# Performance work log

Hardware: AMD Instinct MI355X
Metric: run time of the kernel (lower is better)

The kernel has to match this reference:

```python
import jax, jax.numpy as jnp
import numpy as np

NPERSEG = 128  # filter_size


def setup_inputs() -> dict:
    key = jax.random.key(0)
    x = jax.random.normal(key, (32, 64, 16384), dtype=jnp.float32)
    return {"x": x}


def _welch_psd(x):
    # window=None -> rectangular, scaling = sum(ones^2) = NPERSEG, fs = 1.0
    step = NPERSEG // 2          # noverlap = nperseg // 2
    T = x.shape[-1]
    num_segments = (T - step) // step
    # frame the signal: [B, C, S, NPERSEG]
    idx = jnp.arange(num_segments)[:, None] * step + jnp.arange(NPERSEG)
    segs = x[..., idx]
    segs = segs - jnp.mean(segs, axis=-1, keepdims=True)
    seg_fft = jnp.fft.rfft(segs, axis=-1)
    psd = (jnp.abs(seg_fft) ** 2) / NPERSEG
    # nperseg even -> double all bins except DC and Nyquist
    factor = jnp.ones((psd.shape[-1],), dtype=psd.dtype).at[1:-1].set(2.0)
    psd = psd * factor
    return jnp.mean(psd, axis=-2)  # average over segments -> [B, C, F]


def reference(x):
    psd = _welch_psd(x)                       # [B, C, F], F = 65
    F_bins = psd.shape[-1]
    sqrt_psd = jnp.sqrt(psd)
    # weights = 1 / F (faithful to original: divides by psd.shape[-1])
    barycenter = jnp.sum(sqrt_psd / F_bins, axis=0) ** 2   # [C, F] (first_iter)
    D = jnp.sqrt(barycenter)[None] / sqrt_psd              # [B, C, F]
    H = jnp.fft.irfft(D, axis=-1)                          # [B, C, 2*(F-1)=128]
    H = jnp.fft.fftshift(H, axes=-1)
    H = jnp.flip(H, axis=-1)
    B, C, T = x.shape
    K = H.shape[-1]
    # per-sample depthwise conv1d, padding='same' (torch even-kernel: left=(K-1)//2, right=K-1-left)
    left = (K - 1) // 2
    out = jax.lax.conv_general_dilated(
        x.reshape(1, B * C, T),
        H.reshape(B * C, 1, K),
        window_strides=(1,),
        padding=[(left, K - 1 - left)],
        feature_group_count=B * C,
    )
    return out.reshape(B, C, T)
```

## Files before the change

kernel.cpp:

```cpp
#include <hip/hip_runtime.h>
#include <math.h>

#define NCH   2048
#define TLEN  16384
#define NSEG  255
#define NF    65

typedef __attribute__((ext_vector_type(8))) short bf16x8;
typedef __attribute__((ext_vector_type(4))) float f32x4;

__device__ __forceinline__ unsigned short f2bf(float f) {
    union { float f; unsigned u; } v; v.f = f;
    unsigned r = v.u + 0x7FFF + ((v.u >> 16) & 1);
    return (unsigned short)(r >> 16);
}
__device__ __forceinline__ float bf2f(unsigned short b) {
    union { unsigned u; float f; } v; v.u = ((unsigned)b) << 16;
    return v.f;
}

__device__ __forceinline__ int swzA(int i) {
    return (i & ~63) | ((i & 63) ^ ((i >> 6) & 31));
}
__host__ __device__ constexpr int br6(int i) {
    return ((i & 1) << 5) | ((i & 2) << 3) | ((i & 4) << 1) |
           ((i & 8) >> 1) | ((i & 16) >> 3) | ((i & 32) >> 5);
}

__attribute__((amdgpu_flat_work_group_size(256, 256), amdgpu_waves_per_eu(2, 2)))
__global__ void psd_kernel(const float* __restrict__ x, float* __restrict__ psd_g) {
    __shared__ float xl[TLEN];
    const int ch  = blockIdx.x;
    const int tid = threadIdx.x;
    const int lane = tid & 63;
    const int w    = tid >> 6;
    const float4* __restrict__ x4 = reinterpret_cast<const float4*>(x) + (size_t)ch * (TLEN / 4);
#pragma unroll
    for (int it = 0; it < 16; ++it) {
        int i4 = it * 256 + tid;
        float4 v = x4[i4];
        int i = i4 << 2;
        xl[swzA(i + 0)] = v.x;
        xl[swzA(i + 1)] = v.y;
        xl[swzA(i + 2)] = v.z;
        xl[swzA(i + 3)] = v.w;
    }
    __syncthreads();

    const int   seg   = (tid < NSEG) ? tid : (NSEG - 1);
    const float valid = (tid < NSEG) ? 1.0f : 0.0f;
    const int   base  = seg * 64;

    float zr[64], zi[64];
#pragma unroll
    for (int i = 0; i < 64; ++i) {
        const int rb = br6(i);
        zr[i] = xl[swzA(base + 2 * rb)];
        zi[i] = xl[swzA(base + 2 * rb + 1)];
    }

    constexpr float STR[6] = {-1.0f, 0.0f, 0.70710678f, 0.92387953f, 0.98078528f, 0.99518473f};
    constexpr float STI[6] = {0.0f, -1.0f, -0.70710678f, -0.38268343f, -0.19509032f, -0.09801714f};
#pragma unroll
    for (int st = 0; st < 6; ++st) {
        const int m = 1 << st;
        float wr = 1.0f, wi = 0.0f;
#pragma unroll
        for (int j = 0; j < m; ++j) {
#pragma unroll
            for (int k = 0; k < 64; k += 2 * m) {
                const int a = k + j, b = a + m;
                float tr = wr * zr[b] - wi * zi[b];
                float ti = wr * zi[b] + wi * zr[b];
                zr[b] = zr[a] - tr; zi[b] = zi[a] - ti;
                zr[a] += tr;        zi[a] += ti;
            }
            float nwr = wr * STR[st] - wi * STI[st];
            wi = wr * STI[st] + wi * STR[st];
            wr = nwr;
        }
    }

    float vals[64];
    float p64;
    const float INV128 = 1.0f / 128.0f;
    {
        float v0 = zr[0] + zi[0];
        vals[0] = v0 * v0 * INV128 * valid;
        float v1 = zr[0] - zi[0];
        p64 = v1 * v1 * INV128 * valid;
        vals[32] = (zr[32] * zr[32] + zi[32] * zi[32]) * (2.0f * INV128) * valid;
    }
    float Wr = 0.9987954562f, Wi = -0.0490676743f;
#pragma unroll
    for (int k = 1; k < 32; ++k) {
        float ar = 0.5f * (zr[k] + zr[64 - k]);
        float ai = 0.5f * (zi[k] - zi[64 - k]);
        float br_ = 0.5f * (zi[k] + zi[64 - k]);
        float bi_ = 0.5f * (zr[64 - k] - zr[k]);
        float tr = Wr * br_ - Wi * bi_;
        float ti = Wr * bi_ + Wi * br_;
        float e1r = ar + tr, e1i = ai + ti;
        float e2r = ar - tr, e2i = ai - ti;
        vals[k]      = (e1r * e1r + e1i * e1i) * (2.0f * INV128) * valid;
        vals[64 - k] = (e2r * e2r + e2i * e2i) * (2.0f * INV128) * valid;
        float nWr = Wr * 0.9987954562f - Wi * (-0.0490676743f);
        Wi = Wr * (-0.0490676743f) + Wi * 0.9987954562f;
        Wr = nWr;
    }

    const int l = lane;
#define RSTAGE(m)                                                    \
    {                                                                \
        const bool hi = (l & (m)) != 0;                              \
        _Pragma("unroll")                                            \
        for (int j = 0; j < (m); ++j) {                              \
            float a = vals[j], b = vals[j + (m)];                    \
            float t = __shfl_xor(hi ? a : b, (m));                   \
            vals[j] = (hi ? b : a) + t;                              \
        }                                                            \
    }
    RSTAGE(32) RSTAGE(16) RSTAGE(8) RSTAGE(4) RSTAGE(2) RSTAGE(1)
#undef RSTAGE
    p64 += __shfl_xor(p64, 32);
    p64 += __shfl_xor(p64, 16);
    p64 += __shfl_xor(p64, 8);
    p64 += __shfl_xor(p64, 4);
    p64 += __shfl_xor(p64, 2);
    p64 += __shfl_xor(p64, 1);

    __syncthreads();
    float* red = xl;
    red[w * 80 + lane] = vals[0];
    if (lane == 0) red[320 + w] = p64;
    __syncthreads();
    if (tid < NF) {
        float s;
        if (tid < 64) s = red[tid] + red[80 + tid] + red[160 + tid] + red[240 + tid];
        else          s = red[320] + red[321] + red[322] + red[323];
        psd_g[ch * NF + tid] = s;
    }
}

__launch_bounds__(256)
__global__ void sqrtp_kernel(const float* __restrict__ psd_g, float* __restrict__ sqrtP,
                             float* __restrict__ S) {
    int id = blockIdx.x * 256 + threadIdx.x;
    if (id >= 64 * NF) return;
    int c = id / NF, f = id - c * NF;
    float sum = 0.0f;
    for (int b = 0; b < 32; ++b) {
        int ch = (b << 6) + c;
        float sp = sqrtf(psd_g[ch * NF + f] * (1.0f / 255.0f));
        sqrtP[ch * NF + f] = sp;
        sum += sp;
    }
    S[id] = sum * (1.0f / 65.0f);
}

__launch_bounds__(128)
__global__ void filt_kernel(const float* __restrict__ sqrtP, const float* __restrict__ S,
                            float* __restrict__ h2g) {
    __shared__ float Dl[NF];
    const int ch = blockIdx.x;
    const int c  = ch & 63;
    const int n  = threadIdx.x;
    if (n < NF) {
        if (n == 0) {
            Dl[0] = 32.0f / 65.0f;
        } else {
            float sp = sqrtP[ch * NF + n];
            float sv = S[c * NF + n];
            Dl[n] = (sp > 0.0f) ? sv / sp : 0.0f;
        }
    }
    __syncthreads();
    float sum = Dl[0] + ((n & 1) ? -Dl[64] : Dl[64]);
#pragma unroll
    for (int f = 1; f < 64; ++f) {
        int m = (f * n) & 127;
        sum += 2.0f * Dl[f] * cosf((float)m * 0.04908738521f);
    }
    float h = sum * (1.0f / 128.0f);
    h2g[ch * 128 + ((n + 63) & 127)] = h;
}

#define BS    4096
#define KPAD  160
#define XU    (BS + KPAD)
#define PHYS(u) ((u) + (((u) >> 4) << 2))

__attribute__((amdgpu_flat_work_group_size(256, 256), amdgpu_waves_per_eu(4, 4)))
__global__ void conv_kernel(const float* __restrict__ x, const float* __restrict__ h2g,
                            float* __restrict__ out) {
    __shared__ __align__(16) unsigned short Xh[PHYS(XU)];
    __shared__ __align__(16) unsigned short Xl[PHYS(XU)];
    const int bid  = blockIdx.x;
    const int ch   = bid >> 2;
    const int t0   = (bid & 3) * BS;
    const int tid  = threadIdx.x;
    const int lane = tid & 63;
    const int w    = tid >> 6;
    const float* __restrict__ xrow = x + (size_t)ch * TLEN;

    bf16x8 Ah[5], Al[5];
    {
        const float* __restrict__ hrow = h2g + ch * 128;
        const int r  = lane & 15;
        const int kg = (lane >> 4) << 2;
#pragma unroll
        for (int c = 0; c < 5; ++c) {
#pragma unroll
            for (int e = 0; e < 8; ++e) {
                int idx = 32 * c + kg + (e & 3) + ((e >> 2) << 4) - r - 1;
                float hv = (idx >= 0 && idx < 128) ? hrow[idx] : 0.0f;
                unsigned short hh = f2bf(hv);
                Ah[c][e] = (short)hh;
                Al[c][e] = (short)f2bf(hv - bf2f(hh));
            }
        }
    }

    for (int i4 = tid; i4 < XU / 4; i4 += 256) {
        int u0  = i4 << 2;
        int src = t0 - 64 + u0;
        float4 v;
        if (src >= 0 && src + 3 < TLEN) {
            v = *reinterpret_cast<const float4*>(xrow + src);
        } else {
            v.x = (src + 0 >= 0 && src + 0 < TLEN) ? xrow[src + 0] : 0.0f;
            v.y = (src + 1 >= 0 && src + 1 < TLEN) ? xrow[src + 1] : 0.0f;
            v.z = (src + 2 >= 0 && src + 2 < TLEN) ? xrow[src + 2] : 0.0f;
            v.w = (src + 3 >= 0 && src + 3 < TLEN) ? xrow[src + 3] : 0.0f;
        }
        ushort4 hi, lo;
        hi.x = f2bf(v.x); lo.x = f2bf(v.x - bf2f(hi.x));
        hi.y = f2bf(v.y); lo.y = f2bf(v.y - bf2f(hi.y));
        hi.z = f2bf(v.z); lo.z = f2bf(v.z - bf2f(hi.z));
        hi.w = f2bf(v.w); lo.w = f2bf(v.w - bf2f(hi.w));
        int p = PHYS(u0);
        *reinterpret_cast<ushort4*>(Xh + p) = hi;
        *reinterpret_cast<ushort4*>(Xl + p) = lo;
    }
    __syncthreads();

    const int ub0 = 16 * (lane & 15) + ((lane >> 4) << 2);
#pragma unroll
    for (int q = 0; q < 4; ++q) {
        const int tb = 256 * (w + (q << 2));
        f32x4 acc = {0.0f, 0.0f, 0.0f, 0.0f};
#pragma unroll
        for (int c = 0; c < 5; ++c) {
            int p0 = PHYS(ub0 + tb + 32 * c);
            ushort4 h0 = *reinterpret_cast<const ushort4*>(Xh + p0);
            ushort4 h1 = *reinterpret_cast<const ushort4*>(Xh + p0 + 20);
            ushort4 l0 = *reinterpret_cast<const ushort4*>(Xl + p0);
            ushort4 l1 = *reinterpret_cast<const ushort4*>(Xl + p0 + 20);
            bf16x8 bh = {(short)h0.x, (short)h0.y, (short)h0.z, (short)h0.w,
                         (short)h1.x, (short)h1.y, (short)h1.z, (short)h1.w};
            bf16x8 bl = {(short)l0.x, (short)l0.y, (short)l0.z, (short)l0.w,
                         (short)l1.x, (short)l1.y, (short)l1.z, (short)l1.w};
            acc = __builtin_amdgcn_mfma_f32_16x16x32_bf16(Ah[c], bh, acc, 0, 0, 0);
            acc = __builtin_amdgcn_mfma_f32_16x16x32_bf16(Ah[c], bl, acc, 0, 0, 0);
            acc = __builtin_amdgcn_mfma_f32_16x16x32_bf16(Al[c], bh, acc, 0, 0, 0);
        }
        float* orow = out + (size_t)ch * TLEN + t0 + tb
                    + 16 * (lane & 15) + ((lane >> 4) << 2);
        *reinterpret_cast<float4*>(orow) = make_float4(acc[0], acc[1], acc[2], acc[3]);
    }
}

extern "C" void kernel_launch(void* const* d_in, const int* in_sizes, int n_in,
                              void* d_out, int out_size, void* d_ws, size_t ws_size,
                              hipStream_t stream) {
    (void)in_sizes; (void)n_in; (void)out_size; (void)ws_size;
    const float* x = (const float*)d_in[0];
    float* out = (float*)d_out;
    char* ws = (char*)d_ws;
    float* psd_g = (float*)(ws);
    float* sqrtP = (float*)(ws + 532480);
    float* S     = (float*)(ws + 1064960);
    float* h2g   = (float*)(ws + 1081600);

    psd_kernel <<<NCH,     256, 0, stream>>>(x, psd_g);
    sqrtp_kernel<<<17,     256, 0, stream>>>(psd_g, sqrtP, S);
    filt_kernel<<<NCH,     128, 0, stream>>>(sqrtP, S, h2g);
    conv_kernel<<<NCH * 4, 256, 0, stream>>>(x, h2g, out);
}
```

Measured before the change: 292.6 us.

## Fuse sqrt/barycenter into filter kernel, use cosine table, vectorize LDS ops

Removes the separate sqrtp kernel launch: each filter block recomputes the per-column barycenter sum over 32 batches directly from the PSD buffer. The inverse-DFT loop now reads a shared-memory cosine table instead of calling cosf 63 times per thread. The PSD kernel's LDS stores and loads become float2 accesses with lane swaps that preserve the existing swizzle. This trades a kernel launch and an intermediate buffer for redundant sqrt work in every block (32x per bin).

```diff
diff --git a/kernel.cpp b/kernel.cpp
--- a/kernel.cpp
+++ b/kernel.cpp
@@ -29,7 +29,7 @@
 
 __attribute__((amdgpu_flat_work_group_size(256, 256), amdgpu_waves_per_eu(2, 2)))
 __global__ void psd_kernel(const float* __restrict__ x, float* __restrict__ psd_g) {
-    __shared__ float xl[TLEN];
+    __shared__ __align__(16) float xl[TLEN];
     const int ch  = blockIdx.x;
     const int tid = threadIdx.x;
     const int lane = tid & 63;
@@ -39,11 +39,13 @@
     for (int it = 0; it < 16; ++it) {
         int i4 = it * 256 + tid;
         float4 v = x4[i4];
-        int i = i4 << 2;
-        xl[swzA(i + 0)] = v.x;
-        xl[swzA(i + 1)] = v.y;
-        xl[swzA(i + 2)] = v.z;
-        xl[swzA(i + 3)] = v.w;
+        int i  = i4 << 2;
+        int a0 = swzA(i);
+        const bool sw = ((i >> 6) & 1) != 0;
+        float2 p0 = sw ? make_float2(v.y, v.x) : make_float2(v.x, v.y);
+        float2 p1 = sw ? make_float2(v.w, v.z) : make_float2(v.z, v.w);
+        *reinterpret_cast<float2*>(&xl[a0 & ~1])       = p0;
+        *reinterpret_cast<float2*>(&xl[(a0 ^ 2) & ~1]) = p1;
     }
     __syncthreads();
 
@@ -55,8 +57,11 @@
 #pragma unroll
     for (int i = 0; i < 64; ++i) {
         const int rb = br6(i);
-        zr[i] = xl[swzA(base + 2 * rb)];
-        zi[i] = xl[swzA(base + 2 * rb + 1)];
+        int a = swzA(base + 2 * rb);
+        const float2 v = *reinterpret_cast<const float2*>(&xl[a & ~1]);
+        const bool sw = ((seg ^ i) & 1) != 0;
+        zr[i] = sw ? v.y : v.x;
+        zi[i] = sw ? v.x : v.y;
     }
 
     constexpr float STR[6] = {-1.0f, 0.0f, 0.70710678f, 0.92387953f, 0.98078528f, 0.99518473f};
@@ -142,44 +147,31 @@
     }
 }
 
-__launch_bounds__(256)
-__global__ void sqrtp_kernel(const float* __restrict__ psd_g, float* __restrict__ sqrtP,
-                             float* __restrict__ S) {
-    int id = blockIdx.x * 256 + threadIdx.x;
-    if (id >= 64 * NF) return;
-    int c = id / NF, f = id - c * NF;
-    float sum = 0.0f;
-    for (int b = 0; b < 32; ++b) {
-        int ch = (b << 6) + c;
-        float sp = sqrtf(psd_g[ch * NF + f] * (1.0f / 255.0f));
-        sqrtP[ch * NF + f] = sp;
-        sum += sp;
-    }
-    S[id] = sum * (1.0f / 65.0f);
-}
-
 __launch_bounds__(128)
-__global__ void filt_kernel(const float* __restrict__ sqrtP, const float* __restrict__ S,
-                            float* __restrict__ h2g) {
+__global__ void filt_kernel(const float* __restrict__ psd_g, float* __restrict__ h2g) {
     __shared__ float Dl[NF];
+    __shared__ float cosT[128];
     const int ch = blockIdx.x;
     const int c  = ch & 63;
     const int n  = threadIdx.x;
+    cosT[n] = cosf((float)n * 0.04908738521f);
     if (n < NF) {
         if (n == 0) {
             Dl[0] = 32.0f / 65.0f;
         } else {
-            float sp = sqrtP[ch * NF + n];
-            float sv = S[c * NF + n];
-            Dl[n] = (sp > 0.0f) ? sv / sp : 0.0f;
+            float sp = sqrtf(psd_g[ch * NF + n] * (1.0f / 255.0f));
+            float s = 0.0f;
+            for (int b = 0; b < 32; ++b)
+                s += sqrtf(psd_g[((b << 6) + c) * NF + n] * (1.0f / 255.0f));
+            s *= (1.0f / 65.0f);
+            Dl[n] = (sp > 0.0f) ? s / sp : 0.0f;
         }
     }
     __syncthreads();
     float sum = Dl[0] + ((n & 1) ? -Dl[64] : Dl[64]);
 #pragma unroll
     for (int f = 1; f < 64; ++f) {
-        int m = (f * n) & 127;
-        sum += 2.0f * Dl[f] * cosf((float)m * 0.04908738521f);
+        sum += 2.0f * Dl[f] * cosT[(f * n) & 127];
     }
     float h = sum * (1.0f / 128.0f);
     h2g[ch * 128 + ((n + 63) & 127)] = h;
@@ -278,12 +270,9 @@
     float* out = (float*)d_out;
     char* ws = (char*)d_ws;
     float* psd_g = (float*)(ws);
-    float* sqrtP = (float*)(ws + 532480);
-    float* S     = (float*)(ws + 1064960);
-    float* h2g   = (float*)(ws + 1081600);
+    float* h2g   = (float*)(ws + 532480);
 
     psd_kernel <<<NCH,     256, 0, stream>>>(x, psd_g);
-    sqrtp_kernel<<<17,     256, 0, stream>>>(psd_g, sqrtP, S);
-    filt_kernel<<<NCH,     128, 0, stream>>>(sqrtP, S, h2g);
+    filt_kernel<<<NCH,     128, 0, stream>>>(psd_g, h2g);
     conv_kernel<<<NCH * 4, 256, 0, stream>>>(x, h2g, out);
 }
```

After: 285.5 us. 1.02x faster.
